# Optimization experiments

Hardware: AMD Instinct MI355X
Metric: run time of the kernel (lower is better)

## Reference

```python
import jax, jax.numpy as jnp
import numpy as np

BS, S, DM, H, DK, DV, PRED = 64, 128, 512, 8, 512, 512, 96
NF = S * DM  # Flatten_Head nf = patch_num * d_model
SCALE_INIT = (DM // H) ** (-0.5)  # head_dim from d_model//n_heads per _ScaledDotProductAttention


def setup_inputs() -> dict:
    key = jax.random.key(0)
    ks = jax.random.split(key, 24)
    g = lambda k, shp: (0.02 * jax.random.normal(k, shp)).astype(jnp.float32)
    inp = {
        "x": jax.random.normal(ks[0], (BS, S, DM), dtype=jnp.float32),
        "prev": jax.random.normal(ks[1], (BS, H, S, S), dtype=jnp.float32),
        # multi-head attention projections (d_k = d_v = d_model per TMBlock)
        "Wq": g(ks[2], (DM, H * DK)), "bq": jnp.zeros((H * DK,), jnp.float32),
        "Wk": g(ks[3], (DM, H * DK)), "bk": jnp.zeros((H * DK,), jnp.float32),
        "Wv": g(ks[4], (DM, H * DV)), "bv": jnp.zeros((H * DV,), jnp.float32),
        "Wo": g(ks[5], (H * DV, DM)), "bo": jnp.zeros((DM,), jnp.float32),
        "scale": jnp.float32(SCALE_INIT),
        # InterPatchMixing: Linear(PatchNum, PatchNum) x2
        "Wi1": g(ks[6], (S, S)), "bi1": jnp.zeros((S,), jnp.float32),
        "Wi2": g(ks[7], (S, S)), "bi2": jnp.zeros((S,), jnp.float32),
        # IntraPatchMixing: Linear(PatchEmbedDim, PatchEmbedDim) x2
        "Wt1": g(ks[8], (DM, DM)), "bt1": jnp.zeros((DM,), jnp.float32),
        "Wt2": g(ks[9], (DM, DM)), "bt2": jnp.zeros((DM,), jnp.float32),
        # Flatten_Head (non-individual): Linear(nf, pred_len)
        "Wh": g(ks[10], (NF, PRED)), "bh": jnp.zeros((PRED,), jnp.float32),
    }
    return inp


def reference(x, prev, Wq, bq, Wk, bk, Wv, bv, Wo, bo, scale,
              Wi1, bi1, Wi2, bi2, Wt1, bt1, Wt2, bt2, Wh, bh):
    bs = x.shape[0]
    # projections -> [bs, H, S, d]
    q = (x @ Wq + bq).reshape(bs, S, H, DK).transpose(0, 2, 1, 3)
    k = (x @ Wk + bk).reshape(bs, S, H, DK).transpose(0, 2, 1, 3)
    v = (x @ Wv + bv).reshape(bs, S, H, DV).transpose(0, 2, 1, 3)
    # manual scaled dot-product attention with residual attention bias (Realformer)
    scores = jnp.einsum('bhqd,bhkd->bhqk', q, k) * scale + prev
    attn = jax.nn.softmax(scores, axis=-1)  # dropout is identity at eval
    o = jnp.einsum('bhqk,bhkd->bhqd', attn, v)
    o = o.transpose(0, 2, 1, 3).reshape(bs, S, H * DV)
    o = o @ Wo + bo  # [bs, S, DM]
    # InterPatchMixing over the patch axis (last dim must be PatchNum)
    t = o.transpose(0, 2, 1)  # [bs, DM, S]
    t = jax.nn.relu(t @ Wi1 + bi1) @ Wi2 + bi2
    y = t.transpose(0, 2, 1)  # [bs, S, DM]
    # IntraPatchMixing over embed dim
    z = jax.nn.relu(y @ Wt1 + bt1) @ Wt2 + bt2
    # Flatten_Head: flatten last two dims -> Linear(nf, pred_len)
    out = z.reshape(bs, NF) @ Wh + bh  # [bs, PRED]
    return out
```

## Files before the change

kernel.cpp:

```cpp
#include <hip/hip_runtime.h>
#include <cstdint>
#include <cstddef>

typedef __bf16 bf16_t;
typedef __bf16 bf16x8 __attribute__((ext_vector_type(8)));
typedef __bf16 bf16x4 __attribute__((ext_vector_type(4)));
typedef float  f32x4  __attribute__((ext_vector_type(4)));

#define MFMA(a, b, c) __builtin_amdgcn_mfma_f32_16x16x32_bf16((a), (b), (c), 0, 0, 0)


__global__ __launch_bounds__(256) void k_convert_dual(const float* __restrict__ in,
                                                      bf16_t* __restrict__ xb,
                                                      bf16_t* __restrict__ xT) {
  __shared__ bf16_t tile[32][34];
  int tx = threadIdx.x & 31, ty = threadIdx.x >> 5;
  int c0 = blockIdx.x * 32, r0 = blockIdx.y * 32;
#pragma unroll
  for (int j = 0; j < 4; ++j) {
    int r = r0 + ty + j * 8;
    bf16_t bv = (bf16_t)in[(size_t)r * 512 + c0 + tx];
    xb[(size_t)r * 512 + c0 + tx] = bv;
    tile[ty + j * 8][tx] = bv;
  }
  __syncthreads();
  int b = (r0 + tx) >> 7, s = (r0 + tx) & 127;
#pragma unroll
  for (int j = 0; j < 4; ++j) {
    int i = c0 + ty + j * 8;
    xT[(size_t)b * 65536 + (size_t)i * 128 + s] = tile[tx][ty + j * 8];
  }
}

__global__ __launch_bounds__(256) void k_transpose_convert(const float* __restrict__ in,
                                                           bf16_t* __restrict__ out,
                                                           int R, int C) {
  __shared__ float tile[32][33];
  int tx = threadIdx.x & 31, ty = threadIdx.x >> 5;
  int c0 = blockIdx.x * 32, r0 = blockIdx.y * 32;
#pragma unroll
  for (int j = 0; j < 4; ++j)
    tile[ty + j * 8][tx] = in[(size_t)(r0 + ty + j * 8) * C + c0 + tx];
  __syncthreads();
#pragma unroll
  for (int j = 0; j < 4; ++j)
    out[(size_t)(c0 + ty + j * 8) * R + r0 + tx] = (bf16_t)tile[tx][ty + j * 8];
}

__global__ __launch_bounds__(256) void k_transpose_b16(const bf16_t* __restrict__ in,
                                                       bf16_t* __restrict__ out,
                                                       int R, int C) {
  __shared__ bf16_t tile[32][34];
  size_t base = (size_t)blockIdx.z * R * C;
  int tx = threadIdx.x & 31, ty = threadIdx.x >> 5;
  int c0 = blockIdx.x * 32, r0 = blockIdx.y * 32;
#pragma unroll
  for (int j = 0; j < 4; ++j)
    tile[ty + j * 8][tx] = in[base + (size_t)(r0 + ty + j * 8) * C + c0 + tx];
  __syncthreads();
#pragma unroll
  for (int j = 0; j < 4; ++j)
    out[base + (size_t)(c0 + ty + j * 8) * R + r0 + tx] = tile[tx][ty + j * 8];
}

template <int BMODE>
__global__ __launch_bounds__(256) void k_wprod(const float* __restrict__ Ap,
                                               const float* __restrict__ Bp,
                                               bf16_t* __restrict__ out,
                                               int ldA, int ldB) {
  __shared__ __align__(16) bf16_t As[128 * 68];
  __shared__ __align__(16) bf16_t Bs[128 * 68];
  const int tid = threadIdx.x, lane = tid & 63, wave = tid >> 6;
  const int wr = (wave >> 1) * 64, wc = (wave & 1) * 64;
  const int lr = lane & 15, lk = (lane >> 4) * 8, frow = (lane >> 4) * 4;
  const int m0 = blockIdx.x * 128, n0 = blockIdx.y * 128, h = blockIdx.z;
  const int sr = tid >> 3, sc = (tid & 7) * 8;
  f32x4 acc[4][4] = {};

  for (int kt = 0; kt < 512; kt += 64) {
#pragma unroll
    for (int rr = 0; rr < 4; ++rr) {
      int r = sr + 32 * rr;
      const float* ap = Ap + (size_t)(m0 + r) * ldA + h * 512 + kt + sc;
      bf16x8 av;
#pragma unroll
      for (int e = 0; e < 8; ++e) av[e] = (bf16_t)ap[e];
      *(bf16x8*)(As + r * 68 + sc) = av;
    }
    if (BMODE == 0) {
#pragma unroll
      for (int rr = 0; rr < 4; ++rr) {
        int r = sr + 32 * rr;
        const float* bp = Bp + (size_t)(n0 + r) * ldB + h * 512 + kt + sc;
        bf16x8 bv;
#pragma unroll
        for (int e = 0; e < 8; ++e) bv[e] = (bf16_t)bp[e];
        *(bf16x8*)(Bs + r * 68 + sc) = bv;
      }
    } else {
#pragma unroll
      for (int rr = 0; rr < 8; ++rr) {
        int kr = (tid >> 5) + 8 * rr;
        int nc = (tid & 31) * 4;
        const float* bp = Bp + (size_t)(h * 512 + kt + kr) * ldB + n0 + nc;
        float4 v = *(const float4*)bp;
        Bs[(nc + 0) * 68 + kr] = (bf16_t)v.x;
        Bs[(nc + 1) * 68 + kr] = (bf16_t)v.y;
        Bs[(nc + 2) * 68 + kr] = (bf16_t)v.z;
        Bs[(nc + 3) * 68 + kr] = (bf16_t)v.w;
      }
    }
    __syncthreads();
#pragma unroll
    for (int kk = 0; kk < 2; ++kk) {
      bf16x8 af[4], bfr[4];
#pragma unroll
      for (int i = 0; i < 4; ++i)
        af[i] = *(const bf16x8*)(As + (wr + i * 16 + lr) * 68 + kk * 32 + lk);
#pragma unroll
      for (int j = 0; j < 4; ++j)
        bfr[j] = *(const bf16x8*)(Bs + (wc + j * 16 + lr) * 68 + kk * 32 + lk);
#pragma unroll
      for (int i = 0; i < 4; ++i)
#pragma unroll
        for (int j = 0; j < 4; ++j)
          acc[i][j] = MFMA(af[i], bfr[j], acc[i][j]);
    }
    __syncthreads();
  }
#pragma unroll
  for (int i = 0; i < 4; ++i)
#pragma unroll
    for (int j = 0; j < 4; ++j)
#pragma unroll
      for (int q = 0; q < 4; ++q) {
        int gm = m0 + wr + i * 16 + frow + q;
        int gn = n0 + wc + j * 16 + lr;
        if (BMODE == 0)
          out[(size_t)(h * 512 + gn) * 512 + gm] = (bf16_t)acc[i][j][q];
        else
          out[(size_t)gn * 4096 + h * 512 + gm] = (bf16_t)acc[i][j][q];
      }
}

__global__ __launch_bounds__(256) void k_sbias(const float* __restrict__ Wq,
                                               const float* __restrict__ bk,
                                               const float* __restrict__ Wk,
                                               const float* __restrict__ bq,
                                               float* __restrict__ W1,
                                               float* __restrict__ W2,
                                               float* __restrict__ c) {
  const int lane = threadIdx.x & 63, wave = threadIdx.x >> 6;
  const int i = blockIdx.x * 4 + wave;
  for (int h = 0; h < 8; ++h) {
    float s1 = 0.f, s2 = 0.f;
    for (int d = lane; d < 512; d += 64) {
      s1 += Wq[(size_t)i * 4096 + h * 512 + d] * bk[h * 512 + d];
      s2 += Wk[(size_t)i * 4096 + h * 512 + d] * bq[h * 512 + d];
    }
#pragma unroll
    for (int o = 32; o > 0; o >>= 1) { s1 += __shfl_down(s1, o); s2 += __shfl_down(s2, o); }
    if (lane == 0) { W1[h * 512 + i] = s1; W2[h * 512 + i] = s2; }
  }
  if (blockIdx.x == 0 && wave == 0) {
    for (int h = 0; h < 8; ++h) {
      float cc = 0.f;
      for (int d = lane; d < 512; d += 64) cc += bq[h * 512 + d] * bk[h * 512 + d];
#pragma unroll
      for (int o = 32; o > 0; o >>= 1) cc += __shfl_down(cc, o);
      if (lane == 0) c[h] = cc;
    }
  }
}

__global__ __launch_bounds__(256) void k_tbias(const bf16_t* __restrict__ xb,
                                               const float* __restrict__ W1,
                                               const float* __restrict__ W2,
                                               const float* __restrict__ cb,
                                               float* __restrict__ TallT) {
  __shared__ float Ws[16][512];
  __shared__ float scr[128][32];
  const int tid = threadIdx.x;
  for (int i = tid; i < 4096; i += 256) {
    Ws[i >> 9][i & 511] = W1[i];
    Ws[8 + (i >> 9)][i & 511] = W2[i];
  }
  __syncthreads();
  const int rl = tid & 127, part = tid >> 7;
  const int row = blockIdx.x * 128 + rl;
  const bf16_t* xr = xb + (size_t)row * 512 + part * 256;
  float acc[16] = {};
  for (int i = 0; i < 256; i += 8) {
    bf16x8 xv = *(const bf16x8*)(xr + i);
#pragma unroll
    for (int e = 0; e < 8; ++e) {
      float f = (float)xv[e];
#pragma unroll
      for (int cI = 0; cI < 16; ++cI) acc[cI] += f * Ws[cI][part * 256 + i + e];
    }
  }
#pragma unroll
  for (int cI = 0; cI < 16; ++cI) scr[rl][part * 16 + cI] = acc[cI];
  __syncthreads();
  if (tid < 128) {
    int r = blockIdx.x * 128 + tid;
#pragma unroll
    for (int cI = 0; cI < 16; ++cI) {
      float v = scr[tid][cI] + scr[tid][16 + cI];
      if (cI < 8) v += cb[cI];
      TallT[cI * 8192 + r] = v;
    }
  }
}

__global__ __launch_bounds__(256) void k_cvec1(const float* __restrict__ bv,
                                               const float* __restrict__ Wo,
                                               float* __restrict__ cpart) {
  int cch = blockIdx.x, d = threadIdx.x * 2;
  float ax = 0.f, ay = 0.f;
  for (int n = cch * 128; n < cch * 128 + 128; ++n) {
    float b = bv[n];
    float2 w = *(const float2*)(Wo + (size_t)n * 512 + d);
    ax += b * w.x; ay += b * w.y;
  }
  cpart[(size_t)cch * 512 + d] = ax;
  cpart[(size_t)cch * 512 + d + 1] = ay;
}
__global__ __launch_bounds__(256) void k_cvec2(const float* __restrict__ cpart,
                                               const float* __restrict__ bo,
                                               float* __restrict__ cvec) {
  int d = blockIdx.x * 256 + threadIdx.x;
  float s = bo[d];
  for (int cch = 0; cch < 32; ++cch) s += cpart[(size_t)cch * 512 + d];
  cvec[d] = s;
}

__global__ __launch_bounds__(64, 2) void k_attn5(const bf16_t* __restrict__ xb,
                                                 const bf16_t* __restrict__ xT,
                                                 bf16_t* __restrict__ TU,
                                                 const float* __restrict__ prev,
                                                 const float* __restrict__ scale_p,
                                                 const float* __restrict__ TallT,
                                                 int hg) {
  __shared__ __align__(16) bf16_t Pl[16 * 136];
  __shared__ __align__(16) bf16_t Bw[16 * 72];

  const int lane = threadIdx.x;
  const int lr = lane & 15, lk = (lane >> 4) * 8, frow = (lane >> 4) * 4;
  const int bid = blockIdx.x;
  const int bx = (bid & 7) * 256 + (bid >> 3);
  const int b = bx >> 5, hp = (bx >> 3) & 3, rg = bx & 7;
  const int h = hg * 4 + hp;
  const int r0 = rg * 16;
  const bf16_t* xB = xb + (size_t)b * 65536;
  const bf16_t* xTB = xT + (size_t)b * 65536;
  bf16_t* tB = TU + ((size_t)hp * 8192 + b * 128 + r0) * 512;

  f32x4 sacc[8] = {};
  const bf16_t* aP = tB + (size_t)lr * 512 + lk;
  const bf16_t* bP = xB + (size_t)lr * 512 + lk;
  __builtin_amdgcn_s_setprio(1);
#pragma unroll
  for (int kx = 0; kx < 16; ++kx) {
    bf16x8 af = *(const bf16x8*)(aP + kx * 32);
    bf16x8 bfr[8];
#pragma unroll
    for (int j = 0; j < 8; ++j)
      bfr[j] = *(const bf16x8*)(bP + (size_t)j * 8192 + kx * 32);
#pragma unroll
    for (int j = 0; j < 8; ++j) sacc[j] = MFMA(af, bfr[j], sacc[j]);
  }
  __builtin_amdgcn_s_setprio(0);

  const float scl = scale_p[0];
  const float* t1p = TallT + h * 8192 + b * 128 + r0;
  const float* t2p = TallT + (8 + h) * 8192 + b * 128;
  float t2r[8];
#pragma unroll
  for (int j = 0; j < 8; ++j) t2r[j] = t2p[j * 16 + lr];
#pragma unroll
  for (int e = 0; e < 4; ++e) {
    const int rl = frow + e;
    const float t1 = t1p[rl];
    const float* prow = prev + (((size_t)(b * 8 + h)) * 128 + r0 + rl) * 128;
    float mx = -3.4e38f;
#pragma unroll
    for (int j = 0; j < 8; ++j) {
      float v = scl * (sacc[j][e] + t1 + t2r[j]) + prow[j * 16 + lr];
      sacc[j][e] = v;
      mx = fmaxf(mx, v);
    }
    mx = fmaxf(mx, __shfl_xor(mx, 1));
    mx = fmaxf(mx, __shfl_xor(mx, 2));
    mx = fmaxf(mx, __shfl_xor(mx, 4));
    mx = fmaxf(mx, __shfl_xor(mx, 8));
    float sum = 0.f;
#pragma unroll
    for (int j = 0; j < 8; ++j) {
      float p = __expf(sacc[j][e] - mx);
      sacc[j][e] = p;
      sum += p;
    }
    sum += __shfl_xor(sum, 1);
    sum += __shfl_xor(sum, 2);
    sum += __shfl_xor(sum, 4);
    sum += __shfl_xor(sum, 8);
    float inv = 1.f / sum;
#pragma unroll
    for (int j = 0; j < 8; ++j)
      Pl[rl * 136 + j * 16 + lr] = (bf16_t)(sacc[j][e] * inv);
  }

#pragma unroll
  for (int dc = 0; dc < 8; ++dc) {
    f32x4 oacc[4] = {};
    __builtin_amdgcn_s_setprio(1);
#pragma unroll
    for (int kk = 0; kk < 4; ++kk) {
      bf16x8 pa = *(const bf16x8*)(Pl + lr * 136 + kk * 32 + lk);
      bf16x8 xf[4];
#pragma unroll
      for (int j = 0; j < 4; ++j)
        xf[j] = *(const bf16x8*)(xTB + (size_t)(dc * 64 + j * 16 + lr) * 128 + kk * 32 + lk);
#pragma unroll
      for (int j = 0; j < 4; ++j) oacc[j] = MFMA(pa, xf[j], oacc[j]);
    }
    __builtin_amdgcn_s_setprio(0);
#pragma unroll
    for (int j = 0; j < 4; ++j)
#pragma unroll
      for (int e = 0; e < 4; ++e)
        Bw[(frow + e) * 72 + j * 16 + lr] = (bf16_t)oacc[j][e];
#pragma unroll
    for (int r2 = 0; r2 < 2; ++r2) {
      int row = lane >> 2, chunk = (lane & 3) + r2 * 4;
      *(bf16x8*)(tB + (size_t)row * 512 + dc * 64 + chunk * 8) =
          *(const bf16x8*)(Bw + row * 72 + chunk * 8);
    }
  }
}

template <int OUTMODE, int RELU>
__global__ __launch_bounds__(256) void k_gemm(const bf16_t* __restrict__ A,
                                              const bf16_t* __restrict__ Bt,
                                              const float* __restrict__ bias,
                                              bf16_t* __restrict__ C,
                                              int M, int N, int K) {
  __shared__ __align__(16) bf16_t As[128 * 68];
  __shared__ __align__(16) bf16_t Bs[128 * 68];
  const int tid = threadIdx.x, lane = tid & 63, wave = tid >> 6;
  const int wr = (wave >> 1) * 64, wc = (wave & 1) * 64;
  const int m0 = blockIdx.x * 128, n0 = blockIdx.y * 128;
  const int lr = lane & 15, lk = (lane >> 4) * 8, frow = (lane >> 4) * 4;
  const int sr = tid >> 3, sc = (tid & 7) * 8;
  f32x4 acc[4][4] = {};

  for (int kt = 0; kt < K; kt += 64) {
#pragma unroll
    for (int i = 0; i < 4; ++i) {
      int r = i * 32 + sr;
      *(bf16x8*)(As + r * 68 + sc) = *(const bf16x8*)(A + (size_t)(m0 + r) * K + kt + sc);
      *(bf16x8*)(Bs + r * 68 + sc) = *(const bf16x8*)(Bt + (size_t)(n0 + r) * K + kt + sc);
    }
    __syncthreads();
#pragma unroll
    for (int kk = 0; kk < 2; ++kk) {
      bf16x8 af[4], bfr[4];
#pragma unroll
      for (int i = 0; i < 4; ++i)
        af[i] = *(const bf16x8*)(As + (wr + i * 16 + lr) * 68 + kk * 32 + lk);
#pragma unroll
      for (int j = 0; j < 4; ++j)
        bfr[j] = *(const bf16x8*)(Bs + (wc + j * 16 + lr) * 68 + kk * 32 + lk);
#pragma unroll
      for (int i = 0; i < 4; ++i)
#pragma unroll
        for (int j = 0; j < 4; ++j)
          acc[i][j] = MFMA(af[i], bfr[j], acc[i][j]);
    }
    __syncthreads();
  }
#pragma unroll
  for (int j = 0; j < 4; ++j) {
    int gn = n0 + wc + j * 16 + lr;
    float bv = bias ? bias[gn] : 0.0f;
#pragma unroll
    for (int i = 0; i < 4; ++i) {
#pragma unroll
      for (int q = 0; q < 4; ++q) {
        int gm = m0 + wr + i * 16 + frow + q;
        float v = acc[i][j][q] + bv;
        if (RELU) v = v > 0.0f ? v : 0.0f;
        if (OUTMODE == 0)
          C[(size_t)gm * N + gn] = (bf16_t)v;
        else
          C[((size_t)(gn >> 9) * 8192 + gm) * 512 + (gn & 511)] = (bf16_t)v;
      }
    }
  }
}

template <int MODE>
__global__ __launch_bounds__(256) void k_gemm2(const bf16_t* __restrict__ U,
                                               const bf16_t* __restrict__ bt2,
                                               float* __restrict__ o1acc,
                                               const float* __restrict__ cvec,
                                               bf16_t* __restrict__ o1b, int g) {
  __shared__ __align__(16) bf16_t As[128 * 68];
  __shared__ __align__(16) bf16_t Bs[128 * 68];
  const int tid = threadIdx.x, lane = tid & 63, wave = tid >> 6;
  const int wr = (wave >> 1) * 64, wc = (wave & 1) * 64;
  const int m0 = blockIdx.x * 128, n0 = blockIdx.y * 128;
  const int lr = lane & 15, lk = (lane >> 4) * 8, frow = (lane >> 4) * 4;
  const int sr = tid >> 3, sc = (tid & 7) * 8;
  f32x4 acc[4][4] = {};

  for (int kt = 0; kt < 2048; kt += 64) {
    const int slab = kt >> 9, off = kt & 511;
#pragma unroll
    for (int i = 0; i < 4; ++i) {
      int r = i * 32 + sr;
      *(bf16x8*)(As + r * 68 + sc) =
          *(const bf16x8*)(U + ((size_t)slab * 8192 + m0 + r) * 512 + off + sc);
      *(bf16x8*)(Bs + r * 68 + sc) =
          *(const bf16x8*)(bt2 + (size_t)(n0 + r) * 4096 + g * 2048 + kt + sc);
    }
    __syncthreads();
#pragma unroll
    for (int kk = 0; kk < 2; ++kk) {
      bf16x8 af[4], bfr[4];
#pragma unroll
      for (int i = 0; i < 4; ++i)
        af[i] = *(const bf16x8*)(As + (wr + i * 16 + lr) * 68 + kk * 32 + lk);
#pragma unroll
      for (int j = 0; j < 4; ++j)
        bfr[j] = *(const bf16x8*)(Bs + (wc + j * 16 + lr) * 68 + kk * 32 + lk);
#pragma unroll
      for (int i = 0; i < 4; ++i)
#pragma unroll
        for (int j = 0; j < 4; ++j)
          acc[i][j] = MFMA(af[i], bfr[j], acc[i][j]);
    }
    __syncthreads();
  }
#pragma unroll
  for (int j = 0; j < 4; ++j) {
    int gn = n0 + wc + j * 16 + lr;
#pragma unroll
    for (int i = 0; i < 4; ++i) {
#pragma unroll
      for (int q = 0; q < 4; ++q) {
        int gm = m0 + wr + i * 16 + frow + q;
        size_t idx = (size_t)gm * 512 + gn;
        if (MODE == 0)
          o1acc[idx] = acc[i][j][q];
        else
          o1b[idx] = (bf16_t)(acc[i][j][q] + o1acc[idx] + cvec[gn]);
      }
    }
  }
}

__global__ __launch_bounds__(256) void k_head_partial(const bf16_t* __restrict__ Z,
                                                      const bf16_t* __restrict__ WhT,
                                                      float* __restrict__ part) {
  __shared__ __align__(16) bf16_t As[64 * 68];
  __shared__ __align__(16) bf16_t Bs[96 * 68];
  const int tid = threadIdx.x, lane = tid & 63, wave = tid >> 6;
  const int wr = (wave >> 1) * 32, wc = (wave & 1) * 48;
  const int lr = lane & 15, lk = (lane >> 4) * 8, frow = (lane >> 4) * 4;
  const int k0 = blockIdx.x * 512;
  const int sr = tid >> 3, sc = (tid & 7) * 8;
  f32x4 acc[2][3] = {};
  for (int kt = 0; kt < 512; kt += 64) {
#pragma unroll
    for (int i = 0; i < 2; ++i) {
      int r = i * 32 + sr;
      *(bf16x8*)(As + r * 68 + sc) = *(const bf16x8*)(Z + (size_t)r * 65536 + k0 + kt + sc);
    }
#pragma unroll
    for (int i = 0; i < 3; ++i) {
      int r = i * 32 + sr;
      *(bf16x8*)(Bs + r * 68 + sc) = *(const bf16x8*)(WhT + (size_t)r * 65536 + k0 + kt + sc);
    }
    __syncthreads();
#pragma unroll
    for (int kk = 0; kk < 2; ++kk) {
      bf16x8 af[2], bfr[3];
#pragma unroll
      for (int i = 0; i < 2; ++i)
        af[i] = *(const bf16x8*)(As + (wr + i * 16 + lr) * 68 + kk * 32 + lk);
#pragma unroll
      for (int j = 0; j < 3; ++j)
        bfr[j] = *(const bf16x8*)(Bs + (wc + j * 16 + lr) * 68 + kk * 32 + lk);
#pragma unroll
      for (int i = 0; i < 2; ++i)
#pragma unroll
        for (int j = 0; j < 3; ++j)
          acc[i][j] = MFMA(af[i], bfr[j], acc[i][j]);
    }
    __syncthreads();
  }
#pragma unroll
  for (int i = 0; i < 2; ++i)
#pragma unroll
    for (int j = 0; j < 3; ++j)
#pragma unroll
      for (int q = 0; q < 4; ++q) {
        int m = wr + i * 16 + frow + q;
        int n = wc + j * 16 + lr;
        part[(size_t)blockIdx.x * 6144 + m * 96 + n] = acc[i][j][q];
      }
}

__global__ __launch_bounds__(256) void k_head_reduce(const float* __restrict__ part,
                                                     const float* __restrict__ bias,
                                                     float* __restrict__ out) {
  int idx = blockIdx.x * 256 + threadIdx.x;
  if (idx >= 6144) return;
  float s = bias[idx % 96];
  for (int kb = 0; kb < 128; ++kb) s += part[(size_t)kb * 6144 + idx];
  out[idx] = s;
}

__global__ void k_sentinel(float* out, int n, float val) {
  int i = blockIdx.x * 256 + threadIdx.x;
  if (i < n) out[i] = val;
}

extern "C" void kernel_launch(void* const* d_in, const int* in_sizes, int n_in,
                              void* d_out, int out_size, void* d_ws, size_t ws_size,
                              hipStream_t stream) {
  const float* x    = (const float*)d_in[0];
  const float* prev = (const float*)d_in[1];
  const float* Wq = (const float*)d_in[2];   const float* bq = (const float*)d_in[3];
  const float* Wk = (const float*)d_in[4];   const float* bk = (const float*)d_in[5];
  const float* Wv = (const float*)d_in[6];   const float* bv = (const float*)d_in[7];
  const float* Wo = (const float*)d_in[8];   const float* bo = (const float*)d_in[9];
  const float* scale = (const float*)d_in[10];
  const float* Wi1 = (const float*)d_in[11]; const float* bi1 = (const float*)d_in[12];
  const float* Wi2 = (const float*)d_in[13]; const float* bi2 = (const float*)d_in[14];
  const float* Wt1 = (const float*)d_in[15]; const float* bt1w = (const float*)d_in[16];
  const float* Wt2 = (const float*)d_in[17]; const float* bt2w = (const float*)d_in[18];
  const float* Wh = (const float*)d_in[19];  const float* bh = (const float*)d_in[20];
  float* out = (float*)d_out;

  char* p = (char*)d_ws;
  auto carve = [&](size_t bytes) {
    char* r = p;
    p += (bytes + 255) & ~(size_t)255;
    return r;
  };
  bf16_t* xb    = (bf16_t*)carve((size_t)8192 * 512 * 2);
  bf16_t* xTo1b = (bf16_t*)carve((size_t)8192 * 512 * 2);
  float*  o1acc = (float*)carve((size_t)8192 * 512 * 4);
  bf16_t* bt1   = (bf16_t*)carve((size_t)4096 * 512 * 2);
  bf16_t* bt2   = (bf16_t*)carve((size_t)512 * 4096 * 2);
  float*  W1    = (float*)carve(8 * 512 * 4);
  float*  W2    = (float*)carve(8 * 512 * 4);
  float*  cb    = (float*)carve(8 * 4);
  float*  cvec  = (float*)carve(512 * 4);
  char*   arena = carve((size_t)8192 * 2048 * 2);
  bf16_t* TU    = (bf16_t*)arena;
  float*  cpart = (float*)arena;
  bf16_t* xT    = xTo1b;
  bf16_t* o1b   = xTo1b;
  float*  TallT = (float*)bt1;
  char* q2 = arena;
  auto carve2 = [&](size_t bytes) {
    char* r = q2;
    q2 += (bytes + 255) & ~(size_t)255;
    return r;
  };
  bf16_t* whT  = (bf16_t*)carve2((size_t)96 * 65536 * 2);
  bf16_t* wt1T = (bf16_t*)carve2((size_t)512 * 512 * 2);
  bf16_t* wt2T = (bf16_t*)carve2((size_t)512 * 512 * 2);
  bf16_t* wi1T = (bf16_t*)carve2((size_t)128 * 128 * 2);
  bf16_t* wi2T = (bf16_t*)carve2((size_t)128 * 128 * 2);
  float*  hp   = (float*)carve2((size_t)128 * 64 * 96 * 4);
  bf16_t* bufB = (bf16_t*)carve2((size_t)8192 * 512 * 2);

  if ((size_t)(p - (char*)d_ws) > ws_size) {
    k_sentinel<<<24, 256, 0, stream>>>(out, 6144, (float)ws_size);
    return;
  }

  dim3 blk(256);
  k_cvec1<<<32, blk, 0, stream>>>(bv, Wo, cpart);
  k_cvec2<<<2, blk, 0, stream>>>(cpart, bo, cvec);
  k_convert_dual<<<dim3(16, 256), blk, 0, stream>>>(x, xb, xT);
  k_wprod<0><<<dim3(4, 4, 8), blk, 0, stream>>>(Wq, Wk, bt1, 4096, 4096);
  k_wprod<1><<<dim3(4, 4, 8), blk, 0, stream>>>(Wv, Wo, bt2, 4096, 512);
  k_sbias<<<128, blk, 0, stream>>>(Wq, bk, Wk, bq, W1, W2, cb);

  k_gemm<2, 0><<<dim3(64, 16), blk, 0, stream>>>(xb, bt1, nullptr, TU, 8192, 2048, 512);
  k_tbias<<<64, blk, 0, stream>>>(xb, W1, W2, cb, TallT);
  k_attn5<<<2048, dim3(64), 0, stream>>>(xb, xT, TU, prev, scale, TallT, 0);
  k_gemm2<0><<<dim3(64, 4), blk, 0, stream>>>(TU, bt2, o1acc, cvec, o1b, 0);
  k_gemm<2, 0><<<dim3(64, 16), blk, 0, stream>>>(xb, bt1 + (size_t)2048 * 512, nullptr, TU,
                                                 8192, 2048, 512);
  k_attn5<<<2048, dim3(64), 0, stream>>>(xb, xT, TU, prev, scale, TallT, 1);
  k_gemm2<1><<<dim3(64, 4), blk, 0, stream>>>(TU, bt2, o1acc, cvec, o1b, 1);

  k_transpose_convert<<<dim3(4, 4), blk, 0, stream>>>(Wi1, wi1T, 128, 128);
  k_transpose_convert<<<dim3(4, 4), blk, 0, stream>>>(Wi2, wi2T, 128, 128);
  k_transpose_convert<<<dim3(16, 16), blk, 0, stream>>>(Wt1, wt1T, 512, 512);
  k_transpose_convert<<<dim3(16, 16), blk, 0, stream>>>(Wt2, wt2T, 512, 512);
  k_transpose_convert<<<dim3(3, 2048), blk, 0, stream>>>(Wh, whT, 65536, 96);

  k_transpose_b16<<<dim3(16, 4, 64), blk, 0, stream>>>(o1b, bufB, 128, 512);
  k_gemm<0, 1><<<dim3(256, 1), blk, 0, stream>>>(bufB, wi1T, bi1, o1b, 32768, 128, 128);
  k_gemm<0, 0><<<dim3(256, 1), blk, 0, stream>>>(o1b, wi2T, bi2, bufB, 32768, 128, 128);
  k_transpose_b16<<<dim3(4, 16, 64), blk, 0, stream>>>(bufB, o1b, 512, 128);

  k_gemm<0, 1><<<dim3(64, 4), blk, 0, stream>>>(o1b, wt1T, bt1w, bufB, 8192, 512, 512);
  k_gemm<0, 0><<<dim3(64, 4), blk, 0, stream>>>(bufB, wt2T, bt2w, o1b, 8192, 512, 512);

  k_head_partial<<<128, blk, 0, stream>>>(o1b, whT, hp);
  k_head_reduce<<<24, blk, 0, stream>>>(hp, bh, out);
}
```

Measured before the change: 481.1 us.

## Split attention block across four waves with cross-wave softmax reduction

The attention kernel now runs 256 threads per block instead of one wave. Each wave computes 32 of the 128 key columns of the score tile, and row max and sum are combined across waves through shared-memory scratch with barriers. In the P·V stage each wave handles two of the eight output column chunks. This raises parallelism and occupancy per block and lowers per-wave register pressure, at the cost of three __syncthreads and redundant reloads of the A fragment in every wave.

After: 501.2 us. 1.04x slower.

```diff
diff --git a/kernel.cpp b/kernel.cpp
--- a/kernel.cpp
+++ b/kernel.cpp
@@ -235,17 +235,19 @@
   cvec[d] = s;
 }
 
-__global__ __launch_bounds__(64, 2) void k_attn5(const bf16_t* __restrict__ xb,
-                                                 const bf16_t* __restrict__ xT,
-                                                 bf16_t* __restrict__ TU,
-                                                 const float* __restrict__ prev,
-                                                 const float* __restrict__ scale_p,
-                                                 const float* __restrict__ TallT,
-                                                 int hg) {
+__global__ __launch_bounds__(256, 8) void k_attn6(const bf16_t* __restrict__ xb,
+                                                  const bf16_t* __restrict__ xT,
+                                                  bf16_t* __restrict__ TU,
+                                                  const float* __restrict__ prev,
+                                                  const float* __restrict__ scale_p,
+                                                  const float* __restrict__ TallT,
+                                                  int hg) {
   __shared__ __align__(16) bf16_t Pl[16 * 136];
-  __shared__ __align__(16) bf16_t Bw[16 * 72];
-
-  const int lane = threadIdx.x;
+  __shared__ __align__(16) bf16_t Bw[4][16 * 72];
+  __shared__ float scrM[4][16], scrS[4][16];
+
+  const int tid = threadIdx.x;
+  const int lane = tid & 63, wave = tid >> 6;
   const int lr = lane & 15, lk = (lane >> 4) * 8, frow = (lane >> 4) * 4;
   const int bid = blockIdx.x;
   const int bx = (bid & 7) * 256 + (bid >> 3);
@@ -256,63 +258,82 @@
   const bf16_t* xTB = xT + (size_t)b * 65536;
   bf16_t* tB = TU + ((size_t)hp * 8192 + b * 128 + r0) * 512;
 
-  f32x4 sacc[8] = {};
+  f32x4 sacc[2] = {};
   const bf16_t* aP = tB + (size_t)lr * 512 + lk;
-  const bf16_t* bP = xB + (size_t)lr * 512 + lk;
+  const bf16_t* bP = xB + (size_t)(wave * 32 + lr) * 512 + lk;
   __builtin_amdgcn_s_setprio(1);
 #pragma unroll
   for (int kx = 0; kx < 16; ++kx) {
     bf16x8 af = *(const bf16x8*)(aP + kx * 32);
-    bf16x8 bfr[8];
-#pragma unroll
-    for (int j = 0; j < 8; ++j)
-      bfr[j] = *(const bf16x8*)(bP + (size_t)j * 8192 + kx * 32);
-#pragma unroll
-    for (int j = 0; j < 8; ++j) sacc[j] = MFMA(af, bfr[j], sacc[j]);
+    bf16x8 b0 = *(const bf16x8*)(bP + kx * 32);
+    bf16x8 b1 = *(const bf16x8*)(bP + 16 * 512 + kx * 32);
+    sacc[0] = MFMA(af, b0, sacc[0]);
+    sacc[1] = MFMA(af, b1, sacc[1]);
   }
   __builtin_amdgcn_s_setprio(0);
 
   const float scl = scale_p[0];
   const float* t1p = TallT + h * 8192 + b * 128 + r0;
-  const float* t2p = TallT + (8 + h) * 8192 + b * 128;
-  float t2r[8];
-#pragma unroll
-  for (int j = 0; j < 8; ++j) t2r[j] = t2p[j * 16 + lr];
+  const float* t2p = TallT + (8 + h) * 8192 + b * 128 + wave * 32;
+  float t2r[2];
+  t2r[0] = t2p[lr];
+  t2r[1] = t2p[16 + lr];
+  float mx2[4];
 #pragma unroll
   for (int e = 0; e < 4; ++e) {
     const int rl = frow + e;
     const float t1 = t1p[rl];
-    const float* prow = prev + (((size_t)(b * 8 + h)) * 128 + r0 + rl) * 128;
-    float mx = -3.4e38f;
-#pragma unroll
-    for (int j = 0; j < 8; ++j) {
-      float v = scl * (sacc[j][e] + t1 + t2r[j]) + prow[j * 16 + lr];
-      sacc[j][e] = v;
-      mx = fmaxf(mx, v);
-    }
+    const float* prow = prev + (((size_t)(b * 8 + h)) * 128 + r0 + rl) * 128 + wave * 32;
+    float v0 = scl * (sacc[0][e] + t1 + t2r[0]) + prow[lr];
+    float v1 = scl * (sacc[1][e] + t1 + t2r[1]) + prow[16 + lr];
+    sacc[0][e] = v0;
+    sacc[1][e] = v1;
+    float mx = fmaxf(v0, v1);
     mx = fmaxf(mx, __shfl_xor(mx, 1));
     mx = fmaxf(mx, __shfl_xor(mx, 2));
     mx = fmaxf(mx, __shfl_xor(mx, 4));
     mx = fmaxf(mx, __shfl_xor(mx, 8));
-    float sum = 0.f;
-#pragma unroll
-    for (int j = 0; j < 8; ++j) {
-      float p = __expf(sacc[j][e] - mx);
-      sacc[j][e] = p;
-      sum += p;
-    }
+    mx2[e] = mx;
+  }
+  if ((lane & 15) == 0) {
+#pragma unroll
+    for (int e = 0; e < 4; ++e) scrM[wave][frow + e] = mx2[e];
+  }
+  __syncthreads();
+  float sum2[4];
+#pragma unroll
+  for (int e = 0; e < 4; ++e) {
+    const int rl = frow + e;
+    float mx = fmaxf(fmaxf(scrM[0][rl], scrM[1][rl]), fmaxf(scrM[2][rl], scrM[3][rl]));
+    float p0 = __expf(sacc[0][e] - mx);
+    float p1 = __expf(sacc[1][e] - mx);
+    sacc[0][e] = p0;
+    sacc[1][e] = p1;
+    float sum = p0 + p1;
     sum += __shfl_xor(sum, 1);
     sum += __shfl_xor(sum, 2);
     sum += __shfl_xor(sum, 4);
     sum += __shfl_xor(sum, 8);
-    float inv = 1.f / sum;
-#pragma unroll
-    for (int j = 0; j < 8; ++j)
-      Pl[rl * 136 + j * 16 + lr] = (bf16_t)(sacc[j][e] * inv);
-  }
-
-#pragma unroll
-  for (int dc = 0; dc < 8; ++dc) {
+    sum2[e] = sum;
+  }
+  if ((lane & 15) == 0) {
+#pragma unroll
+    for (int e = 0; e < 4; ++e) scrS[wave][frow + e] = sum2[e];
+  }
+  __syncthreads();
+#pragma unroll
+  for (int e = 0; e < 4; ++e) {
+    const int rl = frow + e;
+    float inv = 1.f / (scrS[0][rl] + scrS[1][rl] + scrS[2][rl] + scrS[3][rl]);
+    Pl[rl * 136 + wave * 32 + lr] = (bf16_t)(sacc[0][e] * inv);
+    Pl[rl * 136 + wave * 32 + 16 + lr] = (bf16_t)(sacc[1][e] * inv);
+  }
+  __syncthreads();
+
+  bf16_t* Bww = Bw[wave];
+#pragma unroll
+  for (int di = 0; di < 2; ++di) {
+    const int dc = wave * 2 + di;
     f32x4 oacc[4] = {};
     __builtin_amdgcn_s_setprio(1);
 #pragma unroll
@@ -330,12 +351,12 @@
     for (int j = 0; j < 4; ++j)
 #pragma unroll
       for (int e = 0; e < 4; ++e)
-        Bw[(frow + e) * 72 + j * 16 + lr] = (bf16_t)oacc[j][e];
+        Bww[(frow + e) * 72 + j * 16 + lr] = (bf16_t)oacc[j][e];
 #pragma unroll
     for (int r2 = 0; r2 < 2; ++r2) {
       int row = lane >> 2, chunk = (lane & 3) + r2 * 4;
       *(bf16x8*)(tB + (size_t)row * 512 + dc * 64 + chunk * 8) =
-          *(const bf16x8*)(Bw + row * 72 + chunk * 8);
+          *(const bf16x8*)(Bww + row * 72 + chunk * 8);
     }
   }
 }
@@ -595,11 +616,11 @@
 
   k_gemm<2, 0><<<dim3(64, 16), blk, 0, stream>>>(xb, bt1, nullptr, TU, 8192, 2048, 512);
   k_tbias<<<64, blk, 0, stream>>>(xb, W1, W2, cb, TallT);
-  k_attn5<<<2048, dim3(64), 0, stream>>>(xb, xT, TU, prev, scale, TallT, 0);
+  k_attn6<<<2048, blk, 0, stream>>>(xb, xT, TU, prev, scale, TallT, 0);
   k_gemm2<0><<<dim3(64, 4), blk, 0, stream>>>(TU, bt2, o1acc, cvec, o1b, 0);
   k_gemm<2, 0><<<dim3(64, 16), blk, 0, stream>>>(xb, bt1 + (size_t)2048 * 512, nullptr, TU,
                                                  8192, 2048, 512);
-  k_attn5<<<2048, dim3(64), 0, stream>>>(xb, xT, TU, prev, scale, TallT, 1);
+  k_attn6<<<2048, blk, 0, stream>>>(xb, xT, TU, prev, scale, TallT, 1);
   k_gemm2<1><<<dim3(64, 4), blk, 0, stream>>>(TU, bt2, o1acc, cvec, o1b, 1);
 
   k_transpose_convert<<<dim3(4, 4), blk, 0, stream>>>(Wi1, wi1T, 128, 128);
```

## Shrink GEMM tiles for more blocks, stage wprod stores through LDS

Applied to the files above, without the earlier changes.

Several small-grid GEMMs (inter/intra patch mixing, the second attention-output GEMM, the flatten head) are relaunched with smaller tiles: a new 64x128 kernel, a 128x64 variant of gemm2 with a re-laid-out bt2, and a head split of 256 instead of 128 K-chunks. Doubling the block count is meant to fill more of the CUs on the device. The wprod weight-product kernel now stages its transposed output through shared memory so the global writes are coalesced 16-byte stores. The trade-off is less data reuse per block, more partial sums to reduce in the head, and extra shared-memory traffic.

New measurement: 494.4 us. 2.8% more time.

```diff
diff --git a/kernel.cpp b/kernel.cpp
--- a/kernel.cpp
+++ b/kernel.cpp
@@ -68,8 +68,9 @@
                                                const float* __restrict__ Bp,
                                                bf16_t* __restrict__ out,
                                                int ldA, int ldB) {
-  __shared__ __align__(16) bf16_t As[128 * 68];
-  __shared__ __align__(16) bf16_t Bs[128 * 68];
+  __shared__ __align__(16) bf16_t S[128 * 68 * 2];
+  bf16_t* As = S;
+  bf16_t* Bs = S + 128 * 68;
   const int tid = threadIdx.x, lane = tid & 63, wave = tid >> 6;
   const int wr = (wave >> 1) * 64, wc = (wave & 1) * 64;
   const int lr = lane & 15, lk = (lane >> 4) * 8, frow = (lane >> 4) * 4;
@@ -128,19 +129,23 @@
     }
     __syncthreads();
   }
+
+  bf16_t* Full = S;
 #pragma unroll
   for (int i = 0; i < 4; ++i)
 #pragma unroll
     for (int j = 0; j < 4; ++j)
 #pragma unroll
-      for (int q = 0; q < 4; ++q) {
-        int gm = m0 + wr + i * 16 + frow + q;
-        int gn = n0 + wc + j * 16 + lr;
-        if (BMODE == 0)
-          out[(size_t)(h * 512 + gn) * 512 + gm] = (bf16_t)acc[i][j][q];
-        else
-          out[(size_t)gn * 4096 + h * 512 + gm] = (bf16_t)acc[i][j][q];
-      }
+      for (int q = 0; q < 4; ++q)
+        Full[(wc + j * 16 + lr) * 136 + wr + i * 16 + frow + q] = (bf16_t)acc[i][j][q];
+  __syncthreads();
+#pragma unroll
+  for (int it = 0; it < 8; ++it) {
+    int r = it * 16 + (tid >> 4);
+    int c = (tid & 15) * 8;
+    *(bf16x8*)(out + ((size_t)(h * 512 + n0 + r)) * 512 + m0 + c) =
+        *(const bf16x8*)(Full + r * 136 + c);
+  }
 }
 
 __global__ __launch_bounds__(256) void k_sbias(const float* __restrict__ Wq,
@@ -400,20 +405,72 @@
   }
 }
 
-template <int MODE>
-__global__ __launch_bounds__(256) void k_gemm2(const bf16_t* __restrict__ U,
-                                               const bf16_t* __restrict__ bt2,
-                                               float* __restrict__ o1acc,
-                                               const float* __restrict__ cvec,
-                                               bf16_t* __restrict__ o1b, int g) {
-  __shared__ __align__(16) bf16_t As[128 * 68];
+template <int RELU>
+__global__ __launch_bounds__(256) void k_gemm64(const bf16_t* __restrict__ A,
+                                                const bf16_t* __restrict__ Bt,
+                                                const float* __restrict__ bias,
+                                                bf16_t* __restrict__ C,
+                                                int M, int N, int K) {
+  __shared__ __align__(16) bf16_t As[64 * 68];
   __shared__ __align__(16) bf16_t Bs[128 * 68];
   const int tid = threadIdx.x, lane = tid & 63, wave = tid >> 6;
-  const int wr = (wave >> 1) * 64, wc = (wave & 1) * 64;
-  const int m0 = blockIdx.x * 128, n0 = blockIdx.y * 128;
+  const int m0 = blockIdx.x * 64, n0 = blockIdx.y * 128;
   const int lr = lane & 15, lk = (lane >> 4) * 8, frow = (lane >> 4) * 4;
   const int sr = tid >> 3, sc = (tid & 7) * 8;
-  f32x4 acc[4][4] = {};
+  f32x4 acc[8] = {};
+
+  for (int kt = 0; kt < K; kt += 64) {
+#pragma unroll
+    for (int i = 0; i < 2; ++i) {
+      int r = i * 32 + sr;
+      *(bf16x8*)(As + r * 68 + sc) = *(const bf16x8*)(A + (size_t)(m0 + r) * K + kt + sc);
+    }
+#pragma unroll
+    for (int i = 0; i < 4; ++i) {
+      int r = i * 32 + sr;
+      *(bf16x8*)(Bs + r * 68 + sc) = *(const bf16x8*)(Bt + (size_t)(n0 + r) * K + kt + sc);
+    }
+    __syncthreads();
+#pragma unroll
+    for (int kk = 0; kk < 2; ++kk) {
+      bf16x8 af = *(const bf16x8*)(As + (wave * 16 + lr) * 68 + kk * 32 + lk);
+      bf16x8 bfr[8];
+#pragma unroll
+      for (int j = 0; j < 8; ++j)
+        bfr[j] = *(const bf16x8*)(Bs + (j * 16 + lr) * 68 + kk * 32 + lk);
+#pragma unroll
+      for (int j = 0; j < 8; ++j) acc[j] = MFMA(af, bfr[j], acc[j]);
+    }
+    __syncthreads();
+  }
+#pragma unroll
+  for (int j = 0; j < 8; ++j) {
+    int gn = n0 + j * 16 + lr;
+    float bv = bias ? bias[gn] : 0.0f;
+#pragma unroll
+    for (int q = 0; q < 4; ++q) {
+      int gm = m0 + wave * 16 + frow + q;
+      float v = acc[j][q] + bv;
+      if (RELU) v = v > 0.0f ? v : 0.0f;
+      C[(size_t)gm * N + gn] = (bf16_t)v;
+    }
+  }
+}
+
+template <int MODE>
+__global__ __launch_bounds__(256) void k_gemm2n(const bf16_t* __restrict__ U,
+                                                const bf16_t* __restrict__ bt2,
+                                                float* __restrict__ o1acc,
+                                                const float* __restrict__ cvec,
+                                                bf16_t* __restrict__ o1b, int g) {
+  __shared__ __align__(16) bf16_t As[128 * 68];
+  __shared__ __align__(16) bf16_t Bs[64 * 68];
+  const int tid = threadIdx.x, lane = tid & 63, wave = tid >> 6;
+  const int wr = (wave >> 1) * 64, wc = (wave & 1) * 32;
+  const int m0 = blockIdx.x * 128, n0 = blockIdx.y * 64;
+  const int lr = lane & 15, lk = (lane >> 4) * 8, frow = (lane >> 4) * 4;
+  const int sr = tid >> 3, sc = (tid & 7) * 8;
+  f32x4 acc[4][2] = {};
 
   for (int kt = 0; kt < 2048; kt += 64) {
     const int slab = kt >> 9, off = kt & 511;
@@ -422,29 +479,33 @@
       int r = i * 32 + sr;
       *(bf16x8*)(As + r * 68 + sc) =
           *(const bf16x8*)(U + ((size_t)slab * 8192 + m0 + r) * 512 + off + sc);
+    }
+#pragma unroll
+    for (int i = 0; i < 2; ++i) {
+      int r = i * 32 + sr;
       *(bf16x8*)(Bs + r * 68 + sc) =
-          *(const bf16x8*)(bt2 + (size_t)(n0 + r) * 4096 + g * 2048 + kt + sc);
+          *(const bf16x8*)(bt2 + ((size_t)(g * 4 + slab) * 512 + n0 + r) * 512 + off + sc);
     }
     __syncthreads();
 #pragma unroll
     for (int kk = 0; kk < 2; ++kk) {
-      bf16x8 af[4], bfr[4];
+      bf16x8 af[4], bfr[2];
 #pragma unroll
       for (int i = 0; i < 4; ++i)
         af[i] = *(const bf16x8*)(As + (wr + i * 16 + lr) * 68 + kk * 32 + lk);
 #pragma unroll
-      for (int j = 0; j < 4; ++j)
+      for (int j = 0; j < 2; ++j)
         bfr[j] = *(const bf16x8*)(Bs + (wc + j * 16 + lr) * 68 + kk * 32 + lk);
 #pragma unroll
       for (int i = 0; i < 4; ++i)
 #pragma unroll
-        for (int j = 0; j < 4; ++j)
+        for (int j = 0; j < 2; ++j)
           acc[i][j] = MFMA(af[i], bfr[j], acc[i][j]);
     }
     __syncthreads();
   }
 #pragma unroll
-  for (int j = 0; j < 4; ++j) {
+  for (int j = 0; j < 2; ++j) {
     int gn = n0 + wc + j * 16 + lr;
 #pragma unroll
     for (int i = 0; i < 4; ++i) {
@@ -469,10 +530,10 @@
   const int tid = threadIdx.x, lane = tid & 63, wave = tid >> 6;
   const int wr = (wave >> 1) * 32, wc = (wave & 1) * 48;
   const int lr = lane & 15, lk = (lane >> 4) * 8, frow = (lane >> 4) * 4;
-  const int k0 = blockIdx.x * 512;
+  const int k0 = blockIdx.x * 256;
   const int sr = tid >> 3, sc = (tid & 7) * 8;
   f32x4 acc[2][3] = {};
-  for (int kt = 0; kt < 512; kt += 64) {
+  for (int kt = 0; kt < 256; kt += 64) {
 #pragma unroll
     for (int i = 0; i < 2; ++i) {
       int r = i * 32 + sr;
@@ -519,7 +580,7 @@
   int idx = blockIdx.x * 256 + threadIdx.x;
   if (idx >= 6144) return;
   float s = bias[idx % 96];
-  for (int kb = 0; kb < 128; ++kb) s += part[(size_t)kb * 6144 + idx];
+  for (int kb = 0; kb < 256; ++kb) s += part[(size_t)kb * 6144 + idx];
   out[idx] = s;
 }
 
@@ -555,7 +616,7 @@
   bf16_t* xTo1b = (bf16_t*)carve((size_t)8192 * 512 * 2);
   float*  o1acc = (float*)carve((size_t)8192 * 512 * 4);
   bf16_t* bt1   = (bf16_t*)carve((size_t)4096 * 512 * 2);
-  bf16_t* bt2   = (bf16_t*)carve((size_t)512 * 4096 * 2);
+  bf16_t* bt2   = (bf16_t*)carve((size_t)4096 * 512 * 2);
   float*  W1    = (float*)carve(8 * 512 * 4);
   float*  W2    = (float*)carve(8 * 512 * 4);
   float*  cb    = (float*)carve(8 * 4);
@@ -577,7 +638,7 @@
   bf16_t* wt2T = (bf16_t*)carve2((size_t)512 * 512 * 2);
   bf16_t* wi1T = (bf16_t*)carve2((size_t)128 * 128 * 2);
   bf16_t* wi2T = (bf16_t*)carve2((size_t)128 * 128 * 2);
-  float*  hp   = (float*)carve2((size_t)128 * 64 * 96 * 4);
+  float*  hp   = (float*)carve2((size_t)256 * 64 * 96 * 4);
   bf16_t* bufB = (bf16_t*)carve2((size_t)8192 * 512 * 2);
 
   if ((size_t)(p - (char*)d_ws) > ws_size) {
@@ -596,11 +657,11 @@
   k_gemm<2, 0><<<dim3(64, 16), blk, 0, stream>>>(xb, bt1, nullptr, TU, 8192, 2048, 512);
   k_tbias<<<64, blk, 0, stream>>>(xb, W1, W2, cb, TallT);
   k_attn5<<<2048, dim3(64), 0, stream>>>(xb, xT, TU, prev, scale, TallT, 0);
-  k_gemm2<0><<<dim3(64, 4), blk, 0, stream>>>(TU, bt2, o1acc, cvec, o1b, 0);
+  k_gemm2n<0><<<dim3(64, 8), blk, 0, stream>>>(TU, bt2, o1acc, cvec, o1b, 0);
   k_gemm<2, 0><<<dim3(64, 16), blk, 0, stream>>>(xb, bt1 + (size_t)2048 * 512, nullptr, TU,
                                                  8192, 2048, 512);
   k_attn5<<<2048, dim3(64), 0, stream>>>(xb, xT, TU, prev, scale, TallT, 1);
-  k_gemm2<1><<<dim3(64, 4), blk, 0, stream>>>(TU, bt2, o1acc, cvec, o1b, 1);
+  k_gemm2n<1><<<dim3(64, 8), blk, 0, stream>>>(TU, bt2, o1acc, cvec, o1b, 1);
 
   k_transpose_convert<<<dim3(4, 4), blk, 0, stream>>>(Wi1, wi1T, 128, 128);
   k_transpose_convert<<<dim3(4, 4), blk, 0, stream>>>(Wi2, wi2T, 128, 128);
@@ -609,13 +670,13 @@
   k_transpose_convert<<<dim3(3, 2048), blk, 0, stream>>>(Wh, whT, 65536, 96);
 
   k_transpose_b16<<<dim3(16, 4, 64), blk, 0, stream>>>(o1b, bufB, 128, 512);
-  k_gemm<0, 1><<<dim3(256, 1), blk, 0, stream>>>(bufB, wi1T, bi1, o1b, 32768, 128, 128);
-  k_gemm<0, 0><<<dim3(256, 1), blk, 0, stream>>>(o1b, wi2T, bi2, bufB, 32768, 128, 128);
+  k_gemm64<1><<<dim3(512, 1), blk, 0, stream>>>(bufB, wi1T, bi1, o1b, 32768, 128, 128);
+  k_gemm64<0><<<dim3(512, 1), blk, 0, stream>>>(o1b, wi2T, bi2, bufB, 32768, 128, 128);
   k_transpose_b16<<<dim3(4, 16, 64), blk, 0, stream>>>(bufB, o1b, 512, 128);
 
-  k_gemm<0, 1><<<dim3(64, 4), blk, 0, stream>>>(o1b, wt1T, bt1w, bufB, 8192, 512, 512);
-  k_gemm<0, 0><<<dim3(64, 4), blk, 0, stream>>>(bufB, wt2T, bt2w, o1b, 8192, 512, 512);
-
-  k_head_partial<<<128, blk, 0, stream>>>(o1b, whT, hp);
+  k_gemm64<1><<<dim3(128, 4), blk, 0, stream>>>(o1b, wt1T, bt1w, bufB, 8192, 512, 512);
+  k_gemm64<0><<<dim3(128, 4), blk, 0, stream>>>(bufB, wt2T, bt2w, o1b, 8192, 512, 512);
+
+  k_head_partial<<<256, blk, 0, stream>>>(o1b, whT, hp);
   k_head_reduce<<<24, blk, 0, stream>>>(hp, bh, out);
 }
```
